# Performance work log

Measured on AMD Instinct MI355X. Metric: run time of the kernel, lower is better.

## Reference

```python
import jax, jax.numpy as jnp
import numpy as np

B, N, I, D, K = 64, 16, 2048, 32, 32  # batch, num_capsule, input_num_capsule, dim_capsule, input_dim_capsule
ROUTINGS = 3
EPS = 1e-07


def squash(s):
    # squared_norm includes per-element eps before the sum, matching torch code
    sq = jnp.sum(s * s + EPS, axis=-1, keepdims=True)
    return sq * s / ((1.0 + sq) * jnp.sqrt(sq))


def setup_inputs() -> dict:
    key = jax.random.key(0)
    kx, kw = jax.random.split(key)
    x = jax.random.normal(kx, (B, I, K), dtype=jnp.float32)
    # xavier_uniform over a [N, I, D, K] tensor: fan_in = D*K (last two dims treated as matrix by torch init? torch treats dim1.. as fan) -- use gain=1 uniform bound per torch's convention: fan_in = I*D*K/... Use simple xavier over (fan_in=K, fan_out=D) receptive field I*N.
    fan_in = I * K
    fan_out = I * D  # torch: fan_in = size(1)*receptive, here just use uniform bound from full-tensor xavier
    bound = float(np.sqrt(6.0 / (fan_in + fan_out)))
    W = jax.random.uniform(kw, (N, I, D, K), minval=-bound, maxval=bound, dtype=jnp.float32)
    return {"x": x, "W": W}


def reference(x, W):
    # u_hat[b,n,i,d] = sum_k W[n,i,d,k] * x[b,i,k]
    u_hat = jnp.einsum('nidk,bik->bnid', W, x)
    b = jnp.zeros((B, N, I), dtype=u_hat.dtype)
    v = None
    for r in range(ROUTINGS):
        c = jax.nn.softmax(b, axis=1)                 # softmax over num_capsule
        s = jnp.einsum('bni,bnid->bnd', c, u_hat)     # [B, N, D]
        v = squash(s)
        if r < ROUTINGS - 1:
            a = jnp.einsum('bnid,bnd->bni', u_hat, v)
            b = b + a
    return v  # [B, N, D]
```

## Files before the change

### kernel.cpp

```cpp
#include <hip/hip_runtime.h>
#include <stdint.h>

#define Bdim 64
#define Ndim 16
#define Idim 2048
#define Ddim 32
#define Kdim 32
#define EPSV 1e-7f

#define TILE_I   8
#define TILES_PB 8
#define NB_Y     (Idim / (TILE_I * TILES_PB))

typedef __attribute__((ext_vector_type(8))) short short8v;
typedef __attribute__((ext_vector_type(4))) float f32x4;

static __device__ __forceinline__ unsigned pk_rne(float a, float b) {
    unsigned ua = __float_as_uint(a);
    unsigned ub = __float_as_uint(b);
    ua = (ua + 0x7fffu + ((ua >> 16) & 1u)) >> 16;
    ub = (ub + 0x7fffu + ((ub >> 16) & 1u)) >> 16;
    return (ua & 0xffffu) | (ub << 16);
}
static __device__ __forceinline__ float bf2f(unsigned us) {
    return __uint_as_float(us << 16);
}

#define GLL16(g, s)                                                              \
    __builtin_amdgcn_global_load_lds(                                            \
        (const __attribute__((address_space(1))) void*)(uintptr_t)(const void*)(g), \
        (__attribute__((address_space(3))) void*)(uintptr_t)(void*)(s), 16, 0, 0)

__global__ __launch_bounds__(256) void pass1_dma(
    const float* __restrict__ W, const float* __restrict__ x,
    unsigned short* __restrict__ uhat, float* __restrict__ s0)
{
    __shared__ float ldsW[2][TILE_I * 1024];

    const int n     = blockIdx.x;
    const int iblk0 = blockIdx.y * (TILE_I * TILES_PB);
    const int tid   = threadIdx.x;
    const int l     = tid & 63;
    const int bcol  = ((tid >> 6) << 4) + (l & 15);
    const int krow  = l >> 4;

    const float* Wblk = W + ((size_t)n * Idim + iblk0) * (Ddim * Kdim);

    f32x4 acc0 = {0.f, 0.f, 0.f, 0.f};
    f32x4 acc1 = {0.f, 0.f, 0.f, 0.f};
    const f32x4 zero = {0.f, 0.f, 0.f, 0.f};

    {
        const float* Wt = Wblk;
        #pragma unroll
        for (int j = 0; j < 8; ++j) {
            const int c = j * 256 + tid;
            const int lc = c & 63, h = (c >> 6) & 1, mt = (c >> 7) & 1, il = c >> 8;
            const float* src = Wt + il * 1024 + ((mt << 4) + (lc & 15)) * 32
                                  + ((lc >> 4) << 3) + (h << 2);
            GLL16(src, &ldsW[0][0] + (size_t)c * 4);
        }
    }

    for (int t = 0; t < TILES_PB; ++t) {
        if (t + 1 < TILES_PB) {
            const float* Wt = Wblk + (size_t)(t + 1) * (TILE_I * 1024);
            float* dst = &ldsW[(t + 1) & 1][0];
            #pragma unroll
            for (int j = 0; j < 8; ++j) {
                const int c = j * 256 + tid;
                const int lc = c & 63, h = (c >> 6) & 1, mt = (c >> 7) & 1, il = c >> 8;
                const float* src = Wt + il * 1024 + ((mt << 4) + (lc & 15)) * 32
                                      + ((lc >> 4) << 3) + (h << 2);
                GLL16(src, dst + (size_t)c * 4);
            }
            asm volatile("s_waitcnt vmcnt(8)" ::: "memory");
        } else {
            asm volatile("s_waitcnt vmcnt(0)" ::: "memory");
        }
        __builtin_amdgcn_s_barrier();
        __builtin_amdgcn_sched_barrier(0);

        const float* lb = &ldsW[t & 1][0];
        const char*  cb = (const char*)lb;
        const int ibase = iblk0 + t * TILE_I;

        #pragma unroll
        for (int il = 0; il < TILE_I; ++il) {
            const int i = ibase + il;
            const float* xp = x + ((size_t)bcol * Idim + i) * Kdim + (krow << 3);
            float4 xa = ((const float4*)xp)[0];
            float4 xb = ((const float4*)xp)[1];

            union { short8v v; unsigned u[4]; } bf, af0, af1;
            bf.u[0] = pk_rne(xa.x, xa.y); bf.u[1] = pk_rne(xa.z, xa.w);
            bf.u[2] = pk_rne(xb.x, xb.y); bf.u[3] = pk_rne(xb.z, xb.w);

            float4 w00 = *(const float4*)(cb + (size_t)((il * 256 + l)       << 4));
            float4 w01 = *(const float4*)(cb + (size_t)((il * 256 + 64 + l)  << 4));
            float4 w10 = *(const float4*)(cb + (size_t)((il * 256 + 128 + l) << 4));
            float4 w11 = *(const float4*)(cb + (size_t)((il * 256 + 192 + l) << 4));
            af0.u[0] = pk_rne(w00.x, w00.y); af0.u[1] = pk_rne(w00.z, w00.w);
            af0.u[2] = pk_rne(w01.x, w01.y); af0.u[3] = pk_rne(w01.z, w01.w);
            af1.u[0] = pk_rne(w10.x, w10.y); af1.u[1] = pk_rne(w10.z, w10.w);
            af1.u[2] = pk_rne(w11.x, w11.y); af1.u[3] = pk_rne(w11.z, w11.w);

            f32x4 c0 = __builtin_amdgcn_mfma_f32_16x16x32_bf16(af0.v, bf.v, zero, 0, 0, 0);
            f32x4 c1 = __builtin_amdgcn_mfma_f32_16x16x32_bf16(af1.v, bf.v, zero, 0, 0, 0);

            const size_t ubase = (((size_t)bcol * Idim + i) * Ndim + n) * Ddim + (krow << 2);
            uint2 p0; p0.x = pk_rne(c0[0], c0[1]); p0.y = pk_rne(c0[2], c0[3]);
            *(uint2*)(uhat + ubase) = p0;
            uint2 p1; p1.x = pk_rne(c1[0], c1[1]); p1.y = pk_rne(c1[2], c1[3]);
            *(uint2*)(uhat + ubase + 16) = p1;

            acc0 += c0;
            acc1 += c1;
        }
        asm volatile("s_waitcnt lgkmcnt(0)" ::: "memory");
        __builtin_amdgcn_s_barrier();
        __builtin_amdgcn_sched_barrier(0);
    }

    float* sp = s0 + ((size_t)bcol * Ndim + n) * Ddim + (krow << 2);
    #pragma unroll
    for (int r = 0; r < 4; ++r) atomicAdd(sp + r, acc0[r]);
    #pragma unroll
    for (int r = 0; r < 4; ++r) atomicAdd(sp + 16 + r, acc1[r]);
}

__global__ __launch_bounds__(256) void pass1_simple(
    const float* __restrict__ W, const float* __restrict__ x,
    unsigned short* __restrict__ uhat, float* __restrict__ s0, int bbase)
{
    const int IB = 16;
    const int n  = blockIdx.x;
    const int i0 = blockIdx.y * IB;
    const int w  = threadIdx.x >> 6;
    const int l  = threadIdx.x & 63;
    const int bcol  = (w << 4) + (l & 15);
    const int bglob = bbase + bcol;
    const int krow  = l >> 4;

    f32x4 acc0 = {0.f,0.f,0.f,0.f}, acc1 = {0.f,0.f,0.f,0.f};
    const f32x4 zero = {0.f,0.f,0.f,0.f};

    for (int ii = 0; ii < IB; ++ii) {
        const int i = i0 + ii;
        const float* xp = x + ((size_t)bglob * Idim + i) * Kdim + (krow << 3);
        float4 xa = ((const float4*)xp)[0];
        float4 xb = ((const float4*)xp)[1];
        union { short8v v; unsigned u[4]; } bf, af0, af1;
        bf.u[0]=pk_rne(xa.x,xa.y); bf.u[1]=pk_rne(xa.z,xa.w);
        bf.u[2]=pk_rne(xb.x,xb.y); bf.u[3]=pk_rne(xb.z,xb.w);

        const float* wbase = W + ((size_t)n * Idim + i) * Ddim * Kdim + (krow << 3);
        const float* wp0 = wbase + (size_t)(l & 15) * Kdim;
        float4 wa = ((const float4*)wp0)[0];
        float4 wb = ((const float4*)wp0)[1];
        af0.u[0]=pk_rne(wa.x,wa.y); af0.u[1]=pk_rne(wa.z,wa.w);
        af0.u[2]=pk_rne(wb.x,wb.y); af0.u[3]=pk_rne(wb.z,wb.w);
        const float* wp1 = wp0 + 16 * Kdim;
        float4 wc = ((const float4*)wp1)[0];
        float4 wd = ((const float4*)wp1)[1];
        af1.u[0]=pk_rne(wc.x,wc.y); af1.u[1]=pk_rne(wc.z,wc.w);
        af1.u[2]=pk_rne(wd.x,wd.y); af1.u[3]=pk_rne(wd.z,wd.w);

        f32x4 c0 = __builtin_amdgcn_mfma_f32_16x16x32_bf16(af0.v, bf.v, zero, 0,0,0);
        f32x4 c1 = __builtin_amdgcn_mfma_f32_16x16x32_bf16(af1.v, bf.v, zero, 0,0,0);

        const size_t ubase = (((size_t)bcol * Idim + i) * Ndim + n) * Ddim + (krow << 2);
        uint2 p0; p0.x=pk_rne(c0[0],c0[1]); p0.y=pk_rne(c0[2],c0[3]);
        *(uint2*)(uhat + ubase) = p0;
        uint2 p1; p1.x=pk_rne(c1[0],c1[1]); p1.y=pk_rne(c1[2],c1[3]);
        *(uint2*)(uhat + ubase + 16) = p1;
        acc0 += c0; acc1 += c1;
    }
    float* sp = s0 + ((size_t)bglob * Ndim + n) * Ddim + (krow << 2);
    #pragma unroll
    for (int r = 0; r < 4; ++r) atomicAdd(sp + r, acc0[r]);
    #pragma unroll
    for (int r = 0; r < 4; ++r) atomicAdd(sp + 16 + r, acc1[r]);
}

template<int FIRST>
__global__ __launch_bounds__(256) void route_kernel(
    const unsigned short* __restrict__ uhat, const float* __restrict__ vin,
    float* __restrict__ bbuf, float* __restrict__ sout, int bbase)
{
    const int bc = blockIdx.x;
    const int it = blockIdx.y;
    const int w = threadIdx.x >> 6;
    const int l = threadIdx.x & 63;
    const int g = l >> 2, q = l & 3;
    const int bglob = bbase + bc;

    const float* vp = vin + ((size_t)bglob * Ndim + g) * Ddim + (q << 3);
    float vreg[8];
    *(float4*)&vreg[0] = ((const float4*)vp)[0];
    *(float4*)&vreg[4] = ((const float4*)vp)[1];

    float sacc[8];
    #pragma unroll
    for (int j = 0; j < 8; ++j) sacc[j] = 0.f;

    for (int ii = w; ii < 128; ii += 4) {
        const int i = (it << 7) + ii;
        const unsigned short* up = uhat + ((size_t)bc * Idim + i) * (Ndim * Ddim) + (l << 3);
        uint4 uraw = *(const uint4*)up;
        float u[8];
        u[0] = bf2f(uraw.x & 0xffffu); u[1] = bf2f(uraw.x >> 16);
        u[2] = bf2f(uraw.y & 0xffffu); u[3] = bf2f(uraw.y >> 16);
        u[4] = bf2f(uraw.z & 0xffffu); u[5] = bf2f(uraw.z >> 16);
        u[6] = bf2f(uraw.w & 0xffffu); u[7] = bf2f(uraw.w >> 16);

        float p = 0.f;
        #pragma unroll
        for (int j = 0; j < 8; ++j) p = fmaf(u[j], vreg[j], p);
        p += __shfl_xor(p, 1);
        p += __shfl_xor(p, 2);

        float logit = p;
        if (FIRST) {
            if (q == 0) bbuf[((size_t)bc * Idim + i) * Ndim + g] = p;
        } else {
            logit += bbuf[((size_t)bc * Idim + i) * Ndim + g];
        }
        float m = logit;
        m = fmaxf(m, __shfl_xor(m, 4));
        m = fmaxf(m, __shfl_xor(m, 8));
        m = fmaxf(m, __shfl_xor(m, 16));
        m = fmaxf(m, __shfl_xor(m, 32));
        float e = __expf(logit - m);
        float z = e;
        z += __shfl_xor(z, 4);
        z += __shfl_xor(z, 8);
        z += __shfl_xor(z, 16);
        z += __shfl_xor(z, 32);
        float c = e / z;

        #pragma unroll
        for (int j = 0; j < 8; ++j) sacc[j] = fmaf(c, u[j], sacc[j]);
    }

    __shared__ float sl[4][512];
    #pragma unroll
    for (int j = 0; j < 8; ++j) sl[w][(l << 3) + j] = sacc[j];
    __syncthreads();
    for (int e2 = threadIdx.x; e2 < 512; e2 += 256) {
        float vsum = sl[0][e2] + sl[1][e2] + sl[2][e2] + sl[3][e2];
        atomicAdd(sout + (size_t)bglob * (Ndim * Ddim) + e2, vsum);
    }
}

__global__ __launch_bounds__(256) void squash_kernel(
    const float* __restrict__ s, float* __restrict__ vout, float scale, int bbase)
{
    const int tid = blockIdx.x * 256 + threadIdx.x;
    const int row = tid >> 5;
    const int d   = tid & 31;
    const size_t off = ((size_t)bbase * Ndim + row) * Ddim + d;
    float sv = s[off] * scale;
    float t = fmaf(sv, sv, EPSV);
    t += __shfl_xor(t, 1);
    t += __shfl_xor(t, 2);
    t += __shfl_xor(t, 4);
    t += __shfl_xor(t, 8);
    t += __shfl_xor(t, 16);
    float vv = sv * t / ((1.f + t) * sqrtf(t));
    vout[off] = vv;
}

extern "C" void kernel_launch(void* const* d_in, const int* in_sizes, int n_in,
                              void* d_out, int out_size, void* d_ws, size_t ws_size,
                              hipStream_t stream)
{
    (void)in_sizes; (void)n_in; (void)out_size;
    const float* x = (const float*)d_in[0];
    const float* W = (const float*)d_in[1];
    float* out = (float*)d_out;

    const size_t snd = (size_t)Bdim * Ndim * Ddim;
    const size_t fixed = 5 * snd * sizeof(float);

    int Bc = 64;
    while (Bc > 16) {
        size_t need = (size_t)Bc * Idim * Ndim * Ddim * 2 + (size_t)Bc * Idim * Ndim * 4 + fixed;
        if (need <= ws_size) break;
        Bc >>= 1;
    }

    char* p = (char*)d_ws;
    unsigned short* uhat = (unsigned short*)p; p += (size_t)Bc * Idim * Ndim * Ddim * 2;
    float* bbuf = (float*)p;                   p += (size_t)Bc * Idim * Ndim * 4;
    float* sbuf = (float*)p;
    float* s0 = sbuf;
    float* s1 = sbuf + snd;
    float* s2 = sbuf + 2 * snd;
    float* v0 = sbuf + 3 * snd;
    float* v1 = sbuf + 4 * snd;

    for (int bbase = 0; bbase < Bdim; bbase += Bc) {
        (void)hipMemsetAsync(sbuf, 0, 3 * snd * sizeof(float), stream);

        if (Bc == 64) {
            pass1_dma<<<dim3(Ndim, NB_Y), 256, 0, stream>>>(W, x, uhat, s0);
        } else {
            pass1_simple<<<dim3(Ndim, Idim / 16), dim3(64 * (Bc / 16)), 0, stream>>>(
                W, x, uhat, s0, bbase);
        }
        squash_kernel<<<dim3(Bc * 2), 256, 0, stream>>>(s0, v0, 1.f / 16.f, bbase);

        route_kernel<1><<<dim3(Bc, Idim / 128), 256, 0, stream>>>(uhat, v0, bbuf, s1, bbase);
        squash_kernel<<<dim3(Bc * 2), 256, 0, stream>>>(s1, v1, 1.f, bbase);

        route_kernel<0><<<dim3(Bc, Idim / 128), 256, 0, stream>>>(uhat, v1, bbuf, s2, bbase);
        squash_kernel<<<dim3(Bc * 2), 256, 0, stream>>>(s2, out, 1.f, bbase);
    }
}
```

Baseline: 203.6 us.

## Pre-convert x to bf16 in i-major layout and DMA it into LDS alongside W

Adds a convert_x kernel that rounds x to bf16 once and transposes it into an [i][b][k] layout in scratch space (reusing bbuf). pass1 now stages both W and x tiles into double-buffered LDS with global_load_lds, replacing the per-lane strided fp32 global x loads and the bf16 conversion that every n-block repeated. The tile shape changes to TILE_I 4 with 16 tiles per block to keep the LDS footprint in bounds. This costs an extra kernel launch plus a pass over x. The wait count of vmcnt(8) is now also applied on the final tile, which has no outstanding prefetch, so the drain there may be incomplete.

```diff
diff --git a/kernel.cpp b/kernel.cpp
--- a/kernel.cpp
+++ b/kernel.cpp
@@ -8,8 +8,8 @@
 #define Kdim 32
 #define EPSV 1e-7f
 
-#define TILE_I   8
-#define TILES_PB 8
+#define TILE_I   4
+#define TILES_PB 16
 #define NB_Y     (Idim / (TILE_I * TILES_PB))
 
 typedef __attribute__((ext_vector_type(8))) short short8v;
@@ -31,11 +31,27 @@
         (const __attribute__((address_space(1))) void*)(uintptr_t)(const void*)(g), \
         (__attribute__((address_space(3))) void*)(uintptr_t)(void*)(s), 16, 0, 0)
 
+__global__ __launch_bounds__(256) void convert_x(
+    const float* __restrict__ x, unsigned short* __restrict__ x2)
+{
+    const int i  = blockIdx.x;
+    const int b  = threadIdx.x >> 2;
+    const int ko = threadIdx.x & 3;
+    const float* src = x + ((size_t)b * Idim + i) * Kdim + (ko << 3);
+    float4 a = ((const float4*)src)[0];
+    float4 c = ((const float4*)src)[1];
+    uint4 o;
+    o.x = pk_rne(a.x, a.y); o.y = pk_rne(a.z, a.w);
+    o.z = pk_rne(c.x, c.y); o.w = pk_rne(c.z, c.w);
+    *(uint4*)(x2 + ((size_t)i * 64 + b) * 32 + (ko << 3)) = o;
+}
+
 __global__ __launch_bounds__(256) void pass1_dma(
-    const float* __restrict__ W, const float* __restrict__ x,
+    const float* __restrict__ W, const unsigned short* __restrict__ x2,
     unsigned short* __restrict__ uhat, float* __restrict__ s0)
 {
-    __shared__ float ldsW[2][TILE_I * 1024];
+    __shared__ float          ldsW[2][TILE_I * 1024];
+    __shared__ unsigned short ldsX[2][TILE_I * 2048];
 
     const int n     = blockIdx.x;
     const int iblk0 = blockIdx.y * (TILE_I * TILES_PB);
@@ -44,62 +60,56 @@
     const int bcol  = ((tid >> 6) << 4) + (l & 15);
     const int krow  = l >> 4;
 
-    const float* Wblk = W + ((size_t)n * Idim + iblk0) * (Ddim * Kdim);
+    const float*          Wblk = W  + ((size_t)n * Idim + iblk0) * (Ddim * Kdim);
+    const unsigned short* Xblk = x2 + (size_t)iblk0 * (64 * 32);
 
     f32x4 acc0 = {0.f, 0.f, 0.f, 0.f};
     f32x4 acc1 = {0.f, 0.f, 0.f, 0.f};
     const f32x4 zero = {0.f, 0.f, 0.f, 0.f};
 
-    {
-        const float* Wt = Wblk;
-        #pragma unroll
-        for (int j = 0; j < 8; ++j) {
-            const int c = j * 256 + tid;
+    auto stage = [&](int t, int buf) {
+        const float* Wt = Wblk + (size_t)t * (TILE_I * 1024);
+        float* dw = &ldsW[buf][0];
+        #pragma unroll
+        for (int j = 0; j < 4; ++j) {
+            const int c  = j * 256 + tid;
             const int lc = c & 63, h = (c >> 6) & 1, mt = (c >> 7) & 1, il = c >> 8;
             const float* src = Wt + il * 1024 + ((mt << 4) + (lc & 15)) * 32
                                   + ((lc >> 4) << 3) + (h << 2);
-            GLL16(src, &ldsW[0][0] + (size_t)c * 4);
-        }
-    }
+            GLL16(src, dw + (size_t)c * 4);
+        }
+        const unsigned short* Xt = Xblk + (size_t)t * (TILE_I * 2048);
+        unsigned short* dx = &ldsX[buf][0];
+        #pragma unroll
+        for (int j = 0; j < 4; ++j) {
+            const int c = j * 256 + tid;
+            GLL16(Xt + (size_t)c * 8, dx + (size_t)c * 8);
+        }
+    };
+
+    stage(0, 0);
 
     for (int t = 0; t < TILES_PB; ++t) {
-        if (t + 1 < TILES_PB) {
-            const float* Wt = Wblk + (size_t)(t + 1) * (TILE_I * 1024);
-            float* dst = &ldsW[(t + 1) & 1][0];
-            #pragma unroll
-            for (int j = 0; j < 8; ++j) {
-                const int c = j * 256 + tid;
-                const int lc = c & 63, h = (c >> 6) & 1, mt = (c >> 7) & 1, il = c >> 8;
-                const float* src = Wt + il * 1024 + ((mt << 4) + (lc & 15)) * 32
-                                      + ((lc >> 4) << 3) + (h << 2);
-                GLL16(src, dst + (size_t)c * 4);
-            }
-            asm volatile("s_waitcnt vmcnt(8)" ::: "memory");
-        } else {
-            asm volatile("s_waitcnt vmcnt(0)" ::: "memory");
-        }
+        if (t + 1 < TILES_PB) stage(t + 1, (t + 1) & 1);
+        asm volatile("s_waitcnt vmcnt(8)" ::: "memory");
         __builtin_amdgcn_s_barrier();
         __builtin_amdgcn_sched_barrier(0);
 
-        const float* lb = &ldsW[t & 1][0];
-        const char*  cb = (const char*)lb;
+        const float*          lw = &ldsW[t & 1][0];
+        const unsigned short* lx = &ldsX[t & 1][0];
         const int ibase = iblk0 + t * TILE_I;
 
         #pragma unroll
         for (int il = 0; il < TILE_I; ++il) {
             const int i = ibase + il;
-            const float* xp = x + ((size_t)bcol * Idim + i) * Kdim + (krow << 3);
-            float4 xa = ((const float4*)xp)[0];
-            float4 xb = ((const float4*)xp)[1];
 
             union { short8v v; unsigned u[4]; } bf, af0, af1;
-            bf.u[0] = pk_rne(xa.x, xa.y); bf.u[1] = pk_rne(xa.z, xa.w);
-            bf.u[2] = pk_rne(xb.x, xb.y); bf.u[3] = pk_rne(xb.z, xb.w);
-
-            float4 w00 = *(const float4*)(cb + (size_t)((il * 256 + l)       << 4));
-            float4 w01 = *(const float4*)(cb + (size_t)((il * 256 + 64 + l)  << 4));
-            float4 w10 = *(const float4*)(cb + (size_t)((il * 256 + 128 + l) << 4));
-            float4 w11 = *(const float4*)(cb + (size_t)((il * 256 + 192 + l) << 4));
+            bf.v = *(const short8v*)(lx + il * 2048 + bcol * 32 + (krow << 3));
+
+            const float4 w00 = *(const float4*)(lw + ((il * 256 + l)       << 2));
+            const float4 w01 = *(const float4*)(lw + ((il * 256 + 64 + l)  << 2));
+            const float4 w10 = *(const float4*)(lw + ((il * 256 + 128 + l) << 2));
+            const float4 w11 = *(const float4*)(lw + ((il * 256 + 192 + l) << 2));
             af0.u[0] = pk_rne(w00.x, w00.y); af0.u[1] = pk_rne(w00.z, w00.w);
             af0.u[2] = pk_rne(w01.x, w01.y); af0.u[3] = pk_rne(w01.z, w01.w);
             af1.u[0] = pk_rne(w10.x, w10.y); af1.u[1] = pk_rne(w10.z, w10.w);
@@ -304,7 +314,9 @@
         (void)hipMemsetAsync(sbuf, 0, 3 * snd * sizeof(float), stream);
 
         if (Bc == 64) {
-            pass1_dma<<<dim3(Ndim, NB_Y), 256, 0, stream>>>(W, x, uhat, s0);
+            unsigned short* x2 = (unsigned short*)bbuf;
+            convert_x<<<dim3(Idim), 256, 0, stream>>>(x, x2);
+            pass1_dma<<<dim3(Ndim, NB_Y), 256, 0, stream>>>(W, x2, uhat, s0);
         } else {
             pass1_simple<<<dim3(Ndim, Idim / 16), dim3(64 * (Bc / 16)), 0, stream>>>(
                 W, x, uhat, s0, bbase);
```

After: 171.3 us. -15.9%, faster.
